# Optimization experiments

Hardware: AMD Instinct MI355X
Metric: run time of the kernel (lower is better)

The kernel has to match this reference:

```python
import jax, jax.numpy as jnp
import numpy as np

B = 524288   # samples
H = 16       # n_neuron[-1] for every node


def setup_inputs() -> dict:
    key = jax.random.key(0)
    ks = jax.random.split(key, 5)

    def w(k, shape, fan_in):
        return jax.random.normal(k, shape, jnp.float32) * (1.0 / np.sqrt(fan_in))

    return {
        "x":  jax.random.normal(ks[0], (B, 16), jnp.float32),
        # level 1: 8 nodes, each Linear(2 -> 16)
        "W1": w(ks[1], (8, 2, H), 2),  "b1": jnp.zeros((8, H), jnp.float32),
        # level 2: 4 nodes, each Linear(32 -> 16)
        "W2": w(ks[2], (4, 2 * H, H), 2 * H), "b2": jnp.zeros((4, H), jnp.float32),
        # level 3: 2 nodes, each Linear(32 -> 16)
        "W3": w(ks[3], (2, 2 * H, H), 2 * H), "b3": jnp.zeros((2, H), jnp.float32),
        # root: Linear(32 -> 16)
        "W4": w(ks[4], (2 * H, H), 2 * H),    "b4": jnp.zeros((H,), jnp.float32),
    }


def reference(x, W1, b1, W2, b2, W3, b3, W4, b4):
    b = x.shape[0]
    # Level 1: each node N1_i consumes leaves (L_{2i}, L_{2i+1}) -> concat == reshape
    h1 = jax.nn.relu(jnp.einsum('bnc,nch->bnh', x.reshape(b, 8, 2), W1) + b1)          # [B,8,16]
    # Level 2: node N2_i consumes concat(N1_{2i}, N1_{2i+1})
    h2 = jax.nn.relu(jnp.einsum('bnc,nch->bnh', h1.reshape(b, 4, 2 * H), W2) + b2)     # [B,4,16]
    # Level 3
    h3 = jax.nn.relu(jnp.einsum('bnc,nch->bnh', h2.reshape(b, 2, 2 * H), W3) + b3)     # [B,2,16]
    # Root N4_0
    out = jax.nn.relu(h3.reshape(b, 2 * H) @ W4 + b4)                                  # [B,16]
    return out
```

## Files before the change

### kernel.cpp

```cpp
#include <hip/hip_runtime.h>
#include <hip/hip_bf16.h>


typedef __attribute__((ext_vector_type(8))) short bf16x8;
typedef __attribute__((ext_vector_type(4))) short bf16x4;
typedef __attribute__((ext_vector_type(4))) float f32x4;

__device__ __forceinline__ short bfr(float f) {
  return (short)__builtin_bit_cast(unsigned short, __float2bfloat16(f));
}
__device__ __forceinline__ float bf2f(short s) {
  unsigned u = ((unsigned)(unsigned short)s) << 16;
  return __builtin_bit_cast(float, u);
}
__device__ __forceinline__ float relu_(float a) { return fmaxf(a, 0.0f); }
__device__ __forceinline__ f32x4 unpk(bf16x4 p) {
  f32x4 c;
#pragma unroll
  for (int r = 0; r < 4; ++r) c[r] = bf2f(p[r]);
  return c;
}

__global__ __launch_bounds__(256, 4) void tree_mlp_mfma5(
    const float* __restrict__ x,
    const float* __restrict__ W1, const float* __restrict__ b1,
    const float* __restrict__ W2, const float* __restrict__ b2,
    const float* __restrict__ W3, const float* __restrict__ b3,
    const float* __restrict__ W4, const float* __restrict__ b4,
    float* __restrict__ out, int ntiles) {
  const int lane = threadIdx.x & 63;
  const int n = lane & 15;
  const int g = lane >> 4;

  const int wpb = blockDim.x >> 6;
  const int gw = blockIdx.x * wpb + (threadIdx.x >> 6);
  const int nw = gridDim.x * wpb;

  bf16x8 w1f[8];
#pragma unroll
  for (int i = 0; i < 8; ++i) {
    bf16x8 f;
#pragma unroll
    for (int j = 0; j < 8; ++j) f[j] = (short)0;
#pragma unroll
    for (int j = 0; j < 4; ++j) {
      int k = 4 * g + j;
      float v = 0.0f;
      if (k == 2 * i)     v = W1[i * 32 + n];
      if (k == 2 * i + 1) v = W1[i * 32 + 16 + n];
      f[j] = bfr(v);
    }
    if (g == 0) f[4] = bfr(b1[i * 16 + n]);
    w1f[i] = f;
  }
  bf16x8 w2f[4]; bf16x4 c2p[4];
#pragma unroll
  for (int i = 0; i < 4; ++i) {
    bf16x8 f;
#pragma unroll
    for (int j = 0; j < 4; ++j) f[j]     = bfr(W2[i * 512 + (4 * g + j) * 16 + n]);
#pragma unroll
    for (int j = 0; j < 4; ++j) f[4 + j] = bfr(W2[i * 512 + (16 + 4 * g + j) * 16 + n]);
    w2f[i] = f;
#pragma unroll
    for (int r = 0; r < 4; ++r) c2p[i][r] = bfr(b2[i * 16 + 4 * g + r]);
  }
  bf16x8 w3f[2]; bf16x4 c3p[2];
#pragma unroll
  for (int i = 0; i < 2; ++i) {
    bf16x8 f;
#pragma unroll
    for (int j = 0; j < 4; ++j) f[j]     = bfr(W3[i * 512 + (4 * g + j) * 16 + n]);
#pragma unroll
    for (int j = 0; j < 4; ++j) f[4 + j] = bfr(W3[i * 512 + (16 + 4 * g + j) * 16 + n]);
    w3f[i] = f;
#pragma unroll
    for (int r = 0; r < 4; ++r) c3p[i][r] = bfr(b3[i * 16 + 4 * g + r]);
  }
  bf16x8 w4f; bf16x4 c4p;
  {
    bf16x8 f;
#pragma unroll
    for (int j = 0; j < 4; ++j) f[j]     = bfr(W4[(4 * g + j) * 16 + n]);
#pragma unroll
    for (int j = 0; j < 4; ++j) f[4 + j] = bfr(W4[(16 + 4 * g + j) * 16 + n]);
    w4f = f;
#pragma unroll
    for (int r = 0; r < 4; ++r) c4p[r] = bfr(b4[4 * g + r]);
  }

  const short bias_slot = (g == 0) ? bfr(1.0f) : (short)0;
  const f32x4* __restrict__ xf = reinterpret_cast<const f32x4*>(x);
  f32x4* __restrict__ of = reinterpret_cast<f32x4*>(out);

  int t = gw;
  if (t >= ntiles) return;

  f32x4 xa = xf[(size_t)(t * 16 + n) * 4 + g];
  f32x4 xb1 = xa;
  if (t + nw < ntiles) xb1 = xf[(size_t)((t + nw) * 16 + n) * 4 + g];

  for (; t < ntiles; t += nw) {
    f32x4 xc = xb1;
    if (t + 2 * nw < ntiles) xc = xf[(size_t)((t + 2 * nw) * 16 + n) * 4 + g];

    bf16x8 xbf;
    xbf[0] = bfr(xa[0]); xbf[1] = bfr(xa[1]);
    xbf[2] = bfr(xa[2]); xbf[3] = bfr(xa[3]);
    xbf[4] = bias_slot; xbf[5] = 0; xbf[6] = 0; xbf[7] = 0;

    const f32x4 zero = {0.f, 0.f, 0.f, 0.f};

    f32x4 a2_0, a2_1, a3_0, a3_1;

#pragma unroll
    for (int half = 0; half < 2; ++half) {
#pragma unroll
      for (int q = 0; q < 2; ++q) {
        const int li = 4 * half + 2 * q;
        f32x4 aL = __builtin_amdgcn_mfma_f32_16x16x32_bf16(w1f[li],     xbf, zero, 0, 0, 0);
        f32x4 aR = __builtin_amdgcn_mfma_f32_16x16x32_bf16(w1f[li + 1], xbf, zero, 0, 0, 0);
        bf16x8 hb;
#pragma unroll
        for (int r = 0; r < 4; ++r) {
          hb[r]     = bfr(relu_(aL[r]));
          hb[4 + r] = bfr(relu_(aR[r]));
        }
        const int l2i = 2 * half + q;
        f32x4 acc = __builtin_amdgcn_mfma_f32_16x16x32_bf16(w2f[l2i], hb, unpk(c2p[l2i]), 0, 0, 0);
        if (q == 0) a2_0 = acc; else a2_1 = acc;
      }
      bf16x8 hb3;
#pragma unroll
      for (int r = 0; r < 4; ++r) {
        hb3[r]     = bfr(relu_(a2_0[r]));
        hb3[4 + r] = bfr(relu_(a2_1[r]));
      }
      f32x4 acc3 = __builtin_amdgcn_mfma_f32_16x16x32_bf16(w3f[half], hb3, unpk(c3p[half]), 0, 0, 0);
      if (half == 0) a3_0 = acc3; else a3_1 = acc3;
    }

    bf16x8 hb4;
#pragma unroll
    for (int r = 0; r < 4; ++r) {
      hb4[r]     = bfr(relu_(a3_0[r]));
      hb4[4 + r] = bfr(relu_(a3_1[r]));
    }
    f32x4 a4 = __builtin_amdgcn_mfma_f32_16x16x32_bf16(w4f, hb4, unpk(c4p), 0, 0, 0);

    f32x4 o;
#pragma unroll
    for (int r = 0; r < 4; ++r) o[r] = relu_(a4[r]);
    __builtin_nontemporal_store(o, &of[(size_t)(t * 16 + n) * 4 + g]);

    xa = xb1;
    xb1 = xc;
  }
}

extern "C" void kernel_launch(void* const* d_in, const int* in_sizes, int n_in,
                              void* d_out, int out_size, void* d_ws, size_t ws_size,
                              hipStream_t stream) {
  const float* x  = (const float*)d_in[0];
  const float* W1 = (const float*)d_in[1];
  const float* b1 = (const float*)d_in[2];
  const float* W2 = (const float*)d_in[3];
  const float* b2 = (const float*)d_in[4];
  const float* W3 = (const float*)d_in[5];
  const float* b3 = (const float*)d_in[6];
  const float* W4 = (const float*)d_in[7];
  const float* b4 = (const float*)d_in[8];
  float* out = (float*)d_out;

  const int ntiles = in_sizes[0] / 256;
  const int block = 256;
  const int grid = 1024;
  tree_mlp_mfma5<<<grid, block, 0, stream>>>(x, W1, b1, W2, b2, W3, b3, W4, b4,
                                             out, ntiles);
}
```

Measured before the change: 25.08 us.

## Process eight contiguous tiles per wave with four-deep register prefetch ring

Each wave now handles a contiguous block of eight tiles per outer iteration instead of striding one tile at a time across the grid. Four input loads are issued up front and refilled as tiles are consumed, deepening memory-level parallelism. Contiguous per-wave access is also meant to improve DRAM locality. The cost is more live registers for the prefetch buffers and a larger unrolled body.

```diff
diff --git a/kernel.cpp b/kernel.cpp
--- a/kernel.cpp
+++ b/kernel.cpp
@@ -21,7 +21,7 @@
   return c;
 }
 
-__global__ __launch_bounds__(256, 4) void tree_mlp_mfma5(
+__global__ __launch_bounds__(256, 4) void tree_mlp_mfma8(
     const float* __restrict__ x,
     const float* __restrict__ W1, const float* __restrict__ b1,
     const float* __restrict__ W2, const float* __restrict__ b2,
@@ -92,69 +92,76 @@
   const short bias_slot = (g == 0) ? bfr(1.0f) : (short)0;
   const f32x4* __restrict__ xf = reinterpret_cast<const f32x4*>(x);
   f32x4* __restrict__ of = reinterpret_cast<f32x4*>(out);
+  const int lo = n * 4 + g;
 
-  int t = gw;
-  if (t >= ntiles) return;
+  const int base = gw * 8;
+  const int bstr = nw * 8;
 
-  f32x4 xa = xf[(size_t)(t * 16 + n) * 4 + g];
-  f32x4 xb1 = xa;
-  if (t + nw < ntiles) xb1 = xf[(size_t)((t + nw) * 16 + n) * 4 + g];
+  for (int b = base; b < ntiles; b += bstr) {
+    f32x4 xw0, xw1, xw2, xw3;
+    xw0 = xf[(size_t)(b) * 64 + lo];
+    if (b + 1 < ntiles) xw1 = xf[(size_t)(b + 1) * 64 + lo];
+    if (b + 2 < ntiles) xw2 = xf[(size_t)(b + 2) * 64 + lo];
+    if (b + 3 < ntiles) xw3 = xf[(size_t)(b + 3) * 64 + lo];
 
-  for (; t < ntiles; t += nw) {
-    f32x4 xc = xb1;
-    if (t + 2 * nw < ntiles) xc = xf[(size_t)((t + 2 * nw) * 16 + n) * 4 + g];
-
-    bf16x8 xbf;
-    xbf[0] = bfr(xa[0]); xbf[1] = bfr(xa[1]);
-    xbf[2] = bfr(xa[2]); xbf[3] = bfr(xa[3]);
-    xbf[4] = bias_slot; xbf[5] = 0; xbf[6] = 0; xbf[7] = 0;
-
-    const f32x4 zero = {0.f, 0.f, 0.f, 0.f};
-
-    f32x4 a2_0, a2_1, a3_0, a3_1;
-
-#pragma unroll
-    for (int half = 0; half < 2; ++half) {
-#pragma unroll
-      for (int q = 0; q < 2; ++q) {
-        const int li = 4 * half + 2 * q;
-        f32x4 aL = __builtin_amdgcn_mfma_f32_16x16x32_bf16(w1f[li],     xbf, zero, 0, 0, 0);
-        f32x4 aR = __builtin_amdgcn_mfma_f32_16x16x32_bf16(w1f[li + 1], xbf, zero, 0, 0, 0);
-        bf16x8 hb;
-#pragma unroll
-        for (int r = 0; r < 4; ++r) {
-          hb[r]     = bfr(relu_(aL[r]));
-          hb[4 + r] = bfr(relu_(aR[r]));
-        }
-        const int l2i = 2 * half + q;
-        f32x4 acc = __builtin_amdgcn_mfma_f32_16x16x32_bf16(w2f[l2i], hb, unpk(c2p[l2i]), 0, 0, 0);
-        if (q == 0) a2_0 = acc; else a2_1 = acc;
-      }
-      bf16x8 hb3;
-#pragma unroll
-      for (int r = 0; r < 4; ++r) {
-        hb3[r]     = bfr(relu_(a2_0[r]));
-        hb3[4 + r] = bfr(relu_(a2_1[r]));
-      }
-      f32x4 acc3 = __builtin_amdgcn_mfma_f32_16x16x32_bf16(w3f[half], hb3, unpk(c3p[half]), 0, 0, 0);
-      if (half == 0) a3_0 = acc3; else a3_1 = acc3;
+#define TILE_STEP(K, SLOT, PREFETCH_STMT)                                      \
+    if (b + (K) < ntiles) {                                                    \
+      f32x4 xv = SLOT;                                                         \
+      PREFETCH_STMT;                                                           \
+      bf16x8 xbf;                                                              \
+      xbf[0] = bfr(xv[0]); xbf[1] = bfr(xv[1]);                                \
+      xbf[2] = bfr(xv[2]); xbf[3] = bfr(xv[3]);                                \
+      xbf[4] = bias_slot; xbf[5] = 0; xbf[6] = 0; xbf[7] = 0;                  \
+      const f32x4 zero = {0.f, 0.f, 0.f, 0.f};                                 \
+      f32x4 a2_0, a2_1, a3_0, a3_1;                                            \
+      _Pragma("unroll")                                                        \
+      for (int half = 0; half < 2; ++half) {                                   \
+        _Pragma("unroll")                                                      \
+        for (int q = 0; q < 2; ++q) {                                          \
+          const int li = 4 * half + 2 * q;                                     \
+          f32x4 aL = __builtin_amdgcn_mfma_f32_16x16x32_bf16(w1f[li],     xbf, zero, 0, 0, 0); \
+          f32x4 aR = __builtin_amdgcn_mfma_f32_16x16x32_bf16(w1f[li + 1], xbf, zero, 0, 0, 0); \
+          bf16x8 hb;                                                           \
+          _Pragma("unroll")                                                    \
+          for (int r = 0; r < 4; ++r) {                                        \
+            hb[r]     = bfr(relu_(aL[r]));                                     \
+            hb[4 + r] = bfr(relu_(aR[r]));                                     \
+          }                                                                    \
+          const int l2i = 2 * half + q;                                        \
+          f32x4 acc = __builtin_amdgcn_mfma_f32_16x16x32_bf16(w2f[l2i], hb, unpk(c2p[l2i]), 0, 0, 0); \
+          if (q == 0) a2_0 = acc; else a2_1 = acc;                             \
+        }                                                                      \
+        bf16x8 hb3;                                                            \
+        _Pragma("unroll")                                                      \
+        for (int r = 0; r < 4; ++r) {                                          \
+          hb3[r]     = bfr(relu_(a2_0[r]));                                    \
+          hb3[4 + r] = bfr(relu_(a2_1[r]));                                    \
+        }                                                                      \
+        f32x4 acc3 = __builtin_amdgcn_mfma_f32_16x16x32_bf16(w3f[half], hb3, unpk(c3p[half]), 0, 0, 0); \
+        if (half == 0) a3_0 = acc3; else a3_1 = acc3;                          \
+      }                                                                        \
+      bf16x8 hb4;                                                              \
+      _Pragma("unroll")                                                        \
+      for (int r = 0; r < 4; ++r) {                                            \
+        hb4[r]     = bfr(relu_(a3_0[r]));                                      \
+        hb4[4 + r] = bfr(relu_(a3_1[r]));                                      \
+      }                                                                        \
+      f32x4 a4 = __builtin_amdgcn_mfma_f32_16x16x32_bf16(w4f, hb4, unpk(c4p), 0, 0, 0); \
+      f32x4 o;                                                                 \
+      _Pragma("unroll")                                                        \
+      for (int r = 0; r < 4; ++r) o[r] = relu_(a4[r]);                         \
+      __builtin_nontemporal_store(o, &of[(size_t)(b + (K)) * 64 + lo]);        \
     }
 
-    bf16x8 hb4;
-#pragma unroll
-    for (int r = 0; r < 4; ++r) {
-      hb4[r]     = bfr(relu_(a3_0[r]));
-      hb4[4 + r] = bfr(relu_(a3_1[r]));
-    }
-    f32x4 a4 = __builtin_amdgcn_mfma_f32_16x16x32_bf16(w4f, hb4, unpk(c4p), 0, 0, 0);
-
-    f32x4 o;
-#pragma unroll
-    for (int r = 0; r < 4; ++r) o[r] = relu_(a4[r]);
-    __builtin_nontemporal_store(o, &of[(size_t)(t * 16 + n) * 4 + g]);
-
-    xa = xb1;
-    xb1 = xc;
+    TILE_STEP(0, xw0, if (b + 4 < ntiles) xw0 = xf[(size_t)(b + 4) * 64 + lo])
+    TILE_STEP(1, xw1, if (b + 5 < ntiles) xw1 = xf[(size_t)(b + 5) * 64 + lo])
+    TILE_STEP(2, xw2, if (b + 6 < ntiles) xw2 = xf[(size_t)(b + 6) * 64 + lo])
+    TILE_STEP(3, xw3, if (b + 7 < ntiles) xw3 = xf[(size_t)(b + 7) * 64 + lo])
+    TILE_STEP(4, xw0, )
+    TILE_STEP(5, xw1, )
+    TILE_STEP(6, xw2, )
+    TILE_STEP(7, xw3, )
+#undef TILE_STEP
   }
 }
 
@@ -175,6 +182,6 @@
   const int ntiles = in_sizes[0] / 256;
   const int block = 256;
   const int grid = 1024;
-  tree_mlp_mfma5<<<grid, block, 0, stream>>>(x, W1, b1, W2, b2, W3, b3, W4, b4,
+  tree_mlp_mfma8<<<grid, block, 0, stream>>>(x, W1, b1, W2, b2, W3, b3, W4, b4,
                                              out, ntiles);
 }
```

Result: slower. 29.15 us (+16.2%).
